# Kernel tuning notes

Hardware: AMD Instinct MI355X
Metric: run time of the kernel (lower is better)

## Reference

```python
import jax, jax.numpy as jnp
import numpy as np
import math

EMBED_DIM = 768
NUM_HEADS = 12
HEAD_DIM = EMBED_DIM // NUM_HEADS
EPS = 1e-6


def setup_inputs() -> dict:
    key = jax.random.key(0)
    ks = jax.random.split(key, 9)
    T, B, N, D = 4, 4, 1024, EMBED_DIM
    s = 0.02
    return {
        "x": jax.random.normal(ks[0], (T, B, N, D), dtype=jnp.float32),
        "Wq": jax.random.normal(ks[1], (D, D), dtype=jnp.float32) * s,
        "bq": jax.random.normal(ks[2], (D,), dtype=jnp.float32) * s,
        "Wk": jax.random.normal(ks[3], (D, D), dtype=jnp.float32) * s,
        "bk": jax.random.normal(ks[4], (D,), dtype=jnp.float32) * s,
        "Wv": jax.random.normal(ks[5], (D, D), dtype=jnp.float32) * s,
        "bv": jax.random.normal(ks[6], (D,), dtype=jnp.float32) * s,
        "Wo": jax.random.normal(ks[7], (D, D), dtype=jnp.float32) * s,
        "bo": jax.random.normal(ks[8], (D,), dtype=jnp.float32) * s,
    }


def _split_heads(y, T, B, N):
    # [T,B,N,D] -> [T,B,H,N,Dh]
    return y.reshape(T, B, N, NUM_HEADS, HEAD_DIM).transpose(0, 1, 3, 2, 4)


def reference(x, Wq, bq, Wk, bk, Wv, bv, Wo, bo):
    T, B, N, D = x.shape
    # q/k/v projections (nn.Linear: x @ W^T + b)
    q = _split_heads(x @ Wq.T + bq, T, B, N)
    k = _split_heads(x @ Wk.T + bk, T, B, N)
    v = _split_heads(x @ Wv.T + bv, T, B, N)
    # scores = q k^T / sqrt(head_dim)
    scores = jnp.einsum("tbhnd,tbhmd->tbhnm", q, k) / math.sqrt(HEAD_DIM)
    # spike-form normalization: relu then L1-normalize along keys
    act = jax.nn.relu(scores)
    attn = act / (act.sum(axis=-1, keepdims=True) + EPS)
    ctx = jnp.einsum("tbhnm,tbhmd->tbhnd", attn, v)
    # merge heads: [T,B,H,N,Dh] -> [T,B,N,D]
    out = ctx.transpose(0, 1, 3, 2, 4).reshape(T, B, N, D)
    return out @ Wo.T + bo
```

## Files before the change

kernel.cpp:

```cpp
#include <hip/hip_runtime.h>
#include <hip/hip_bf16.h>
#include <cstdint>


typedef __attribute__((ext_vector_type(8))) short short8;
typedef __attribute__((ext_vector_type(4))) float float4v;

__device__ __forceinline__ unsigned short f2bf(float f) {
  unsigned int u = __float_as_uint(f);
  u = (u + 0x7fffu + ((u >> 16) & 1u)) >> 16;
  return (unsigned short)u;
}

__device__ __forceinline__ void gld_lds16(const void* g, void* lds) {
  __builtin_amdgcn_global_load_lds(
      (__attribute__((address_space(1))) void*)(uintptr_t)g,
      (__attribute__((address_space(3))) void*)(uint32_t)(uintptr_t)lds,
      16, 0, 0);
}

__global__ __launch_bounds__(256) void cast4(const float* __restrict__ src,
                                             unsigned short* __restrict__ dst,
                                             int n4) {
  int i = blockIdx.x * 256 + threadIdx.x;
  if (i >= n4) return;
  float4 f = reinterpret_cast<const float4*>(src)[i];
  ushort4 o;
  o.x = f2bf(f.x); o.y = f2bf(f.y); o.z = f2bf(f.z); o.w = f2bf(f.w);
  reinterpret_cast<ushort4*>(dst)[i] = o;
}

template <bool OUT_BF16>
__global__ __launch_bounds__(256) void gemm_bt(
    const unsigned short* __restrict__ A,
    const unsigned short* __restrict__ Bt,
    unsigned short* __restrict__ Cb,
    float* __restrict__ Cf,
    const float* __restrict__ b0, const float* __restrict__ b1,
    const float* __restrict__ b2, int N) {
  constexpr int K = 768;
  __shared__ unsigned short As[128 * 32];
  __shared__ unsigned short Bs[128 * 32];

  const int tid = threadIdx.x;
  const int lane = tid & 63;
  const int w = tid >> 6;
  const int wrow = w >> 1, wcol = w & 1;
  const int l15 = lane & 15, quad = lane >> 4;
  const int i0 = blockIdx.y * 128, j0 = blockIdx.x * 128;

  const unsigned short* ga = A + (size_t)(i0 + 32 * w + (lane >> 2)) * K + (lane & 3) * 8;
  const unsigned short* gb = Bt + (size_t)(j0 + 32 * w + (lane >> 2)) * K + (lane & 3) * 8;

  float4v acc[4][4];
#pragma unroll
  for (int a = 0; a < 4; ++a)
#pragma unroll
    for (int b = 0; b < 4; ++b) acc[a][b] = float4v{0.f, 0.f, 0.f, 0.f};

#pragma unroll 1
  for (int kt = 0; kt < K / 32; ++kt) {
    const unsigned short* pa = ga + kt * 32;
    const unsigned short* pb = gb + kt * 32;
    gld_lds16(pa, &As[(32 * w) * 32]);
    gld_lds16(pa + 16 * K, &As[(32 * w + 16) * 32]);
    gld_lds16(pb, &Bs[(32 * w) * 32]);
    gld_lds16(pb + 16 * K, &Bs[(32 * w + 16) * 32]);
    __syncthreads();

    short8 af[4], bfr[4];
#pragma unroll
    for (int a = 0; a < 4; ++a)
      af[a] = *(const short8*)&As[(wrow * 64 + a * 16 + l15) * 32 + quad * 8];
#pragma unroll
    for (int b = 0; b < 4; ++b)
      bfr[b] = *(const short8*)&Bs[(wcol * 64 + b * 16 + l15) * 32 + quad * 8];
#pragma unroll
    for (int a = 0; a < 4; ++a)
#pragma unroll
      for (int b = 0; b < 4; ++b)
        acc[a][b] = __builtin_amdgcn_mfma_f32_16x16x32_bf16(af[a], bfr[b], acc[a][b], 0, 0, 0);
    __syncthreads();
  }

  const int sel = j0 / 768;
  const float* bp = (sel == 0) ? b0 : ((sel == 1) ? b1 : b2);
#pragma unroll
  for (int a = 0; a < 4; ++a) {
    const int row0 = i0 + wrow * 64 + a * 16 + quad * 4;
#pragma unroll
    for (int b = 0; b < 4; ++b) {
      const int col = j0 + wcol * 64 + b * 16 + l15;
      const float bias = bp[col - sel * 768];
#pragma unroll
      for (int r = 0; r < 4; ++r) {
        const float v = acc[a][b][r] + bias;
        if (OUT_BF16)
          Cb[(size_t)(row0 + r) * N + col] = f2bf(v);
        else
          Cf[(size_t)(row0 + r) * N + col] = v;
      }
    }
  }
}

__global__ __launch_bounds__(256) void transpose_v(
    const unsigned short* __restrict__ qkv, unsigned short* __restrict__ vt) {
  __shared__ unsigned short T[64 * 72];
  const int bz = blockIdx.x;
  const int nt = bz & 15;
  const int tbh = bz >> 4;
  const int tb = tbh / 12, h = tbh % 12;
  const int tid = threadIdx.x;
#pragma unroll
  for (int it = 0; it < 2; ++it) {
    int c = tid + it * 256;
    int row = c >> 3, d0 = (c & 7) * 8;
    const unsigned short* g =
        qkv + (size_t)(tb * 1024 + nt * 64 + row) * 2304 + 1536 + h * 64 + d0;
    *(uint4*)&T[row * 72 + d0] = *(const uint4*)g;
  }
  __syncthreads();
#pragma unroll
  for (int it = 0; it < 2; ++it) {
    int c = tid + it * 256;
    int d = c >> 3, n0 = (c & 7) * 8;
    unsigned short tmp[8];
#pragma unroll
    for (int i = 0; i < 8; ++i) tmp[i] = T[(n0 + i) * 72 + d];
    *(uint4*)&vt[((size_t)(tb * 12 + h) * 64 + d) * 1024 + nt * 64 + n0] =
        *(uint4*)tmp;
  }
}

__global__ __launch_bounds__(256) void attn(
    const unsigned short* __restrict__ qkv,
    const unsigned short* __restrict__ vt,
    unsigned short* __restrict__ ctx) {
  __shared__ unsigned short Qs[64 * 72];
  __shared__ unsigned short Ks[64 * 72];
  __shared__ unsigned short Vs[64 * 72];
  __shared__ unsigned short Ps[4 * 16 * 72];

  const int qt = blockIdx.x;
  const int tbh = blockIdx.y;
  const int tb = tbh / 12, h = tbh % 12;
  const int tid = threadIdx.x, lane = tid & 63, w = tid >> 6;
  const int l15 = lane & 15, quad = lane >> 4;

#pragma unroll
  for (int it = 0; it < 2; ++it) {
    int c = tid + it * 256;
    int row = c >> 3, d0 = (c & 7) * 8;
    const unsigned short* g =
        qkv + (size_t)(tb * 1024 + qt * 64 + row) * 2304 + h * 64 + d0;
    *(uint4*)&Qs[row * 72 + d0] = *(const uint4*)g;
  }
  __syncthreads();
  short8 qf[2];
#pragma unroll
  for (int c = 0; c < 2; ++c)
    qf[c] = *(const short8*)&Qs[(w * 16 + l15) * 72 + c * 32 + quad * 8];

  float4v octx[4];
#pragma unroll
  for (int b = 0; b < 4; ++b) octx[b] = float4v{0.f, 0.f, 0.f, 0.f};
  float den[4] = {0.f, 0.f, 0.f, 0.f};
  unsigned short* Psw = &Ps[w * 16 * 72];

#pragma unroll 1
  for (int kv = 0; kv < 16; ++kv) {
    __syncthreads();
#pragma unroll
    for (int it = 0; it < 2; ++it) {
      int c = tid + it * 256;
      int row = c >> 3, d0 = (c & 7) * 8;
      *(uint4*)&Ks[row * 72 + d0] = *(const uint4*)(
          qkv + (size_t)(tb * 1024 + kv * 64 + row) * 2304 + 768 + h * 64 + d0);
      *(uint4*)&Vs[row * 72 + d0] = *(const uint4*)(
          vt + ((size_t)(tb * 12 + h) * 64 + row) * 1024 + kv * 64 + d0);
    }
    __syncthreads();

    float4v sa[4];
#pragma unroll
    for (int s = 0; s < 4; ++s) sa[s] = float4v{0.f, 0.f, 0.f, 0.f};
#pragma unroll
    for (int s = 0; s < 4; ++s)
#pragma unroll
      for (int c = 0; c < 2; ++c) {
        short8 kf = *(const short8*)&Ks[(s * 16 + l15) * 72 + c * 32 + quad * 8];
        sa[s] = __builtin_amdgcn_mfma_f32_16x16x32_bf16(qf[c], kf, sa[s], 0, 0, 0);
      }

#pragma unroll
    for (int s = 0; s < 4; ++s)
#pragma unroll
      for (int r = 0; r < 4; ++r) {
        float v = sa[s][r];
        v = v > 0.f ? v : 0.f;
        den[r] += v;
        Psw[(quad * 4 + r) * 72 + s * 16 + l15] = f2bf(v);
      }

#pragma unroll
    for (int c = 0; c < 2; ++c) {
      short8 pf = *(const short8*)&Psw[l15 * 72 + c * 32 + quad * 8];
#pragma unroll
      for (int b = 0; b < 4; ++b) {
        short8 vf = *(const short8*)&Vs[(b * 16 + l15) * 72 + c * 32 + quad * 8];
        octx[b] = __builtin_amdgcn_mfma_f32_16x16x32_bf16(pf, vf, octx[b], 0, 0, 0);
      }
    }
  }

#pragma unroll
  for (int r = 0; r < 4; ++r) {
    float d = den[r];
    d += __shfl_xor(d, 1);
    d += __shfl_xor(d, 2);
    d += __shfl_xor(d, 4);
    d += __shfl_xor(d, 8);
    den[r] = 1.f / (d + 8e-6f);
  }

#pragma unroll
  for (int b = 0; b < 4; ++b)
#pragma unroll
    for (int r = 0; r < 4; ++r) {
      const int row = tb * 1024 + qt * 64 + w * 16 + quad * 4 + r;
      const int col = h * 64 + b * 16 + l15;
      ctx[(size_t)row * 768 + col] = f2bf(octx[b][r] * den[r]);
    }
}

extern "C" void kernel_launch(void* const* d_in, const int* in_sizes, int n_in,
                              void* d_out, int out_size, void* d_ws, size_t ws_size,
                              hipStream_t stream) {
  const float* x  = (const float*)d_in[0];
  const float* Wq = (const float*)d_in[1];
  const float* bq = (const float*)d_in[2];
  const float* Wk = (const float*)d_in[3];
  const float* bk = (const float*)d_in[4];
  const float* Wv = (const float*)d_in[5];
  const float* bv = (const float*)d_in[6];
  const float* Wo = (const float*)d_in[7];
  const float* bo = (const float*)d_in[8];
  float* out = (float*)d_out;

  char* ws = (char*)d_ws;
  unsigned short* XBF  = (unsigned short*)(ws);
  unsigned short* CTX  = (unsigned short*)(ws);
  unsigned short* WQKV = (unsigned short*)(ws + 25165824);
  unsigned short* WOb  = (unsigned short*)(ws + 28704768);
  unsigned short* QKV  = (unsigned short*)(ws + 29884416);
  unsigned short* VT   = (unsigned short*)(ws + 105381888);

  cast4<<<12288, 256, 0, stream>>>(x, XBF, 3145728);
  cast4<<<576, 256, 0, stream>>>(Wq, WQKV, 147456);
  cast4<<<576, 256, 0, stream>>>(Wk, WQKV + 589824, 147456);
  cast4<<<576, 256, 0, stream>>>(Wv, WQKV + 1179648, 147456);
  cast4<<<576, 256, 0, stream>>>(Wo, WOb, 147456);

  gemm_bt<true><<<dim3(18, 128), 256, 0, stream>>>(XBF, WQKV, QKV, nullptr,
                                                   bq, bk, bv, 2304);
  transpose_v<<<3072, 256, 0, stream>>>(QKV, VT);
  attn<<<dim3(16, 192), 256, 0, stream>>>(QKV, VT, CTX);
  gemm_bt<false><<<dim3(6, 128), 256, 0, stream>>>(CTX, WOb, nullptr, out,
                                                   bo, bo, bo, 768);
}
```

Baseline: 352.7 us.

## Rewrite attention kernel with 32x32 MFMA tiles and 128-row query blocks

The attention kernel now uses 32x32x16 bf16 MFMAs and gives each wave 32 query rows, so a block covers 128 queries and the grid is halved. Each K/V tile loaded into LDS is therefore reused across twice as many queries. It also computes S^T (K as the A operand), which lets each lane pack pairs of bf16 values with a cheaper conversion and write the P tile with wider stores into the reused Q buffer. The cost is fewer blocks, more accumulator registers per thread, and a round-to-nearest conversion that no longer breaks ties to even.

Result: faster. 342.9 us (-2.8%).

```diff
diff --git a/kernel.cpp b/kernel.cpp
--- a/kernel.cpp
+++ b/kernel.cpp
@@ -5,11 +5,18 @@
 
 typedef __attribute__((ext_vector_type(8))) short short8;
 typedef __attribute__((ext_vector_type(4))) float float4v;
+typedef __attribute__((ext_vector_type(16))) float float16v;
 
 __device__ __forceinline__ unsigned short f2bf(float f) {
   unsigned int u = __float_as_uint(f);
   u = (u + 0x7fffu + ((u >> 16) & 1u)) >> 16;
   return (unsigned short)u;
+}
+
+__device__ __forceinline__ unsigned int pkbf(float a, float b) {
+  unsigned int ua = __float_as_uint(a) + 0x8000u;
+  unsigned int ub = __float_as_uint(b) + 0x8000u;
+  return __builtin_amdgcn_perm(ub, ua, 0x07060302u);
 }
 
 __device__ __forceinline__ void gld_lds16(const void* g, void* lds) {
@@ -133,104 +140,106 @@
   }
 }
 
-__global__ __launch_bounds__(256) void attn(
+__global__ __launch_bounds__(256) void attn32(
     const unsigned short* __restrict__ qkv,
     const unsigned short* __restrict__ vt,
     unsigned short* __restrict__ ctx) {
-  __shared__ unsigned short Qs[64 * 72];
+  __shared__ unsigned short QP[128 * 72];
   __shared__ unsigned short Ks[64 * 72];
   __shared__ unsigned short Vs[64 * 72];
-  __shared__ unsigned short Ps[4 * 16 * 72];
 
   const int qt = blockIdx.x;
   const int tbh = blockIdx.y;
   const int tb = tbh / 12, h = tbh % 12;
   const int tid = threadIdx.x, lane = tid & 63, w = tid >> 6;
-  const int l15 = lane & 15, quad = lane >> 4;
-
-#pragma unroll
-  for (int it = 0; it < 2; ++it) {
-    int c = tid + it * 256;
-    int row = c >> 3, d0 = (c & 7) * 8;
-    const unsigned short* g =
-        qkv + (size_t)(tb * 1024 + qt * 64 + row) * 2304 + h * 64 + d0;
-    *(uint4*)&Qs[row * 72 + d0] = *(const uint4*)g;
-  }
-  __syncthreads();
-  short8 qf[2];
-#pragma unroll
-  for (int c = 0; c < 2; ++c)
-    qf[c] = *(const short8*)&Qs[(w * 16 + l15) * 72 + c * 32 + quad * 8];
-
-  float4v octx[4];
-#pragma unroll
-  for (int b = 0; b < 4; ++b) octx[b] = float4v{0.f, 0.f, 0.f, 0.f};
-  float den[4] = {0.f, 0.f, 0.f, 0.f};
-  unsigned short* Psw = &Ps[w * 16 * 72];
+  const int l31 = lane & 31, hl = lane >> 5;
+
+#pragma unroll
+  for (int it = 0; it < 4; ++it) {
+    int c = it * 256 + tid;
+    int row = c >> 3, col = (c & 7) * 8;
+    *(uint4*)&QP[row * 72 + col] = *(const uint4*)(
+        qkv + (size_t)(tb * 1024 + qt * 128 + row) * 2304 + h * 64 + col);
+  }
+  __syncthreads();
+
+  short8 qf[4];
+#pragma unroll
+  for (int kc = 0; kc < 4; ++kc)
+    qf[kc] = *(const short8*)&QP[(w * 32 + l31) * 72 + kc * 16 + hl * 8];
+  unsigned short* PW = &QP[(w * 32) * 72];
+
+  float16v octx[2];
+#pragma unroll
+  for (int i = 0; i < 16; ++i) { octx[0][i] = 0.f; octx[1][i] = 0.f; }
+  float den = 0.f;
 
 #pragma unroll 1
   for (int kv = 0; kv < 16; ++kv) {
     __syncthreads();
 #pragma unroll
     for (int it = 0; it < 2; ++it) {
-      int c = tid + it * 256;
-      int row = c >> 3, d0 = (c & 7) * 8;
-      *(uint4*)&Ks[row * 72 + d0] = *(const uint4*)(
-          qkv + (size_t)(tb * 1024 + kv * 64 + row) * 2304 + 768 + h * 64 + d0);
-      *(uint4*)&Vs[row * 72 + d0] = *(const uint4*)(
-          vt + ((size_t)(tb * 12 + h) * 64 + row) * 1024 + kv * 64 + d0);
-    }
-    __syncthreads();
-
-    float4v sa[4];
-#pragma unroll
-    for (int s = 0; s < 4; ++s) sa[s] = float4v{0.f, 0.f, 0.f, 0.f};
-#pragma unroll
-    for (int s = 0; s < 4; ++s)
-#pragma unroll
-      for (int c = 0; c < 2; ++c) {
-        short8 kf = *(const short8*)&Ks[(s * 16 + l15) * 72 + c * 32 + quad * 8];
-        sa[s] = __builtin_amdgcn_mfma_f32_16x16x32_bf16(qf[c], kf, sa[s], 0, 0, 0);
-      }
-
-#pragma unroll
-    for (int s = 0; s < 4; ++s)
-#pragma unroll
-      for (int r = 0; r < 4; ++r) {
-        float v = sa[s][r];
-        v = v > 0.f ? v : 0.f;
-        den[r] += v;
-        Psw[(quad * 4 + r) * 72 + s * 16 + l15] = f2bf(v);
-      }
-
-#pragma unroll
-    for (int c = 0; c < 2; ++c) {
-      short8 pf = *(const short8*)&Psw[l15 * 72 + c * 32 + quad * 8];
-#pragma unroll
-      for (int b = 0; b < 4; ++b) {
-        short8 vf = *(const short8*)&Vs[(b * 16 + l15) * 72 + c * 32 + quad * 8];
-        octx[b] = __builtin_amdgcn_mfma_f32_16x16x32_bf16(pf, vf, octx[b], 0, 0, 0);
-      }
-    }
-  }
-
-#pragma unroll
-  for (int r = 0; r < 4; ++r) {
-    float d = den[r];
-    d += __shfl_xor(d, 1);
-    d += __shfl_xor(d, 2);
-    d += __shfl_xor(d, 4);
-    d += __shfl_xor(d, 8);
-    den[r] = 1.f / (d + 8e-6f);
-  }
-
-#pragma unroll
-  for (int b = 0; b < 4; ++b)
-#pragma unroll
-    for (int r = 0; r < 4; ++r) {
-      const int row = tb * 1024 + qt * 64 + w * 16 + quad * 4 + r;
-      const int col = h * 64 + b * 16 + l15;
-      ctx[(size_t)row * 768 + col] = f2bf(octx[b][r] * den[r]);
+      int c = it * 256 + tid;
+      int row = c >> 3, col = (c & 7) * 8;
+      *(uint4*)&Ks[row * 72 + col] = *(const uint4*)(
+          qkv + (size_t)(tb * 1024 + kv * 64 + row) * 2304 + 768 + h * 64 + col);
+      *(uint4*)&Vs[row * 72 + col] = *(const uint4*)(
+          vt + ((size_t)(tb * 12 + h) * 64 + row) * 1024 + kv * 64 + col);
+    }
+    __syncthreads();
+
+#pragma unroll
+    for (int mt = 0; mt < 2; ++mt) {
+      float16v st;
+#pragma unroll
+      for (int i = 0; i < 16; ++i) st[i] = 0.f;
+#pragma unroll
+      for (int kc = 0; kc < 4; ++kc) {
+        short8 af = *(const short8*)&Ks[(mt * 32 + l31) * 72 + kc * 16 + hl * 8];
+        st = __builtin_amdgcn_mfma_f32_32x32x16_bf16(af, qf[kc], st, 0, 0, 0);
+      }
+#pragma unroll
+      for (int g = 0; g < 4; ++g) {
+        float v0 = st[4 * g + 0]; v0 = v0 > 0.f ? v0 : 0.f;
+        float v1 = st[4 * g + 1]; v1 = v1 > 0.f ? v1 : 0.f;
+        float v2 = st[4 * g + 2]; v2 = v2 > 0.f ? v2 : 0.f;
+        float v3 = st[4 * g + 3]; v3 = v3 > 0.f ? v3 : 0.f;
+        den += (v0 + v1) + (v2 + v3);
+        uint2 u;
+        u.x = pkbf(v0, v1);
+        u.y = pkbf(v2, v3);
+        *(uint2*)&PW[l31 * 72 + mt * 32 + g * 8 + hl * 4] = u;
+      }
+    }
+
+    short8 pa[4];
+#pragma unroll
+    for (int kc = 0; kc < 4; ++kc)
+      pa[kc] = *(const short8*)&PW[l31 * 72 + kc * 16 + hl * 8];
+#pragma unroll
+    for (int dt = 0; dt < 2; ++dt)
+#pragma unroll
+      for (int kc = 0; kc < 4; ++kc) {
+        short8 vb = *(const short8*)&Vs[(dt * 32 + l31) * 72 + kc * 16 + hl * 8];
+        octx[dt] = __builtin_amdgcn_mfma_f32_32x32x16_bf16(pa[kc], vb, octx[dt], 0, 0, 0);
+      }
+  }
+
+  den += __shfl_xor(den, 32);
+  __syncthreads();
+  float* dsc = (float*)Ks;
+  if (hl == 0) dsc[w * 32 + l31] = 1.f / (den + 8e-6f);
+  __syncthreads();
+
+#pragma unroll
+  for (int dt = 0; dt < 2; ++dt)
+#pragma unroll
+    for (int reg = 0; reg < 16; ++reg) {
+      const int qrow = (reg & 3) + 8 * (reg >> 2) + 4 * hl;
+      const float sc = dsc[w * 32 + qrow];
+      const int grow = tb * 1024 + qt * 128 + w * 32 + qrow;
+      ctx[(size_t)grow * 768 + h * 64 + dt * 32 + l31] =
+          f2bf(octx[dt][reg] * sc);
     }
 }
 
@@ -265,7 +274,7 @@
   gemm_bt<true><<<dim3(18, 128), 256, 0, stream>>>(XBF, WQKV, QKV, nullptr,
                                                    bq, bk, bv, 2304);
   transpose_v<<<3072, 256, 0, stream>>>(QKV, VT);
-  attn<<<dim3(16, 192), 256, 0, stream>>>(QKV, VT, CTX);
+  attn32<<<dim3(8, 192), 256, 0, stream>>>(QKV, VT, CTX);
   gemm_bt<false><<<dim3(6, 128), 256, 0, stream>>>(CTX, WOb, nullptr, out,
                                                    bo, bo, bo, 768);
 }
```
